# Optimization experiments

Hardware: AMD Instinct MI355X
Metric: run time of the kernel (lower is better)

The kernel has to match this reference:

```python
import jax, jax.numpy as jnp
import numpy as np
from jax import lax

B, L, V = 128, 64, 8192
E = H = 128
STEPS = 10
MAX_BIN = 512
BETA_START, BETA_END = 1e-4, 2e-2


def setup_inputs():
    key = jax.random.key(0)
    k = jax.random.split(key, 23)
    s = 0.05
    padded_x = (jax.random.uniform(k[0], (B, L, V)) < 0.01).astype(jnp.float32)
    lengths = jax.random.randint(k[1], (B,), 1, L + 1)
    visit_mask = (jnp.arange(L)[None, :] < lengths[:, None]).astype(jnp.float32)
    padded_bins = jnp.sort(jax.random.randint(k[2], (B, L), 0, MAX_BIN), axis=1)
    t_diff = jax.random.randint(k[3], (B,), 1, STEPS + 1)
    eps = jax.random.normal(k[4], (B, L, E))
    z0 = jax.random.normal(k[5], (B, L, E))
    noise = jax.random.normal(k[6], (STEPS, B, L, E))
    W_visit = jax.random.normal(k[7], (E, V)) * s
    bin_embed = (jax.random.normal(k[8], (MAX_BIN + 2, E)) * s).at[0].set(0.0)  # padding_idx=0
    W_ih = jax.random.normal(k[9], (4 * H, E)) * s
    W_hh = jax.random.normal(k[10], (4 * H, H)) * s
    b_ih = jax.random.normal(k[11], (4 * H,)) * s
    b_hh = jax.random.normal(k[12], (4 * H,)) * s
    W_cls = jax.random.normal(k[13], (1, H)) * s
    b_cls = jax.random.normal(k[14], (1,)) * s
    W_proj = jax.random.normal(k[15], (E, H)) * s
    time_embed = jax.random.normal(k[16], (STEPS + 1, E)) * s
    W_fuse = jax.random.normal(k[17], (2, 2 * E)) * s
    b_fuse = jax.random.normal(k[18], (2,)) * s
    W_e1 = jax.random.normal(k[19], (E, 2 * E)) * s
    b_e1 = jax.random.normal(k[20], (E,)) * s
    W_e2 = jax.random.normal(k[21], (E, E)) * s
    b_e2 = jax.random.normal(k[22], (E,)) * s
    return dict(padded_x=padded_x, visit_mask=visit_mask, padded_bins=padded_bins,
                t_diff=t_diff, eps=eps, z0=z0, noise=noise, W_visit=W_visit,
                bin_embed=bin_embed, W_ih=W_ih, W_hh=W_hh, b_ih=b_ih, b_hh=b_hh,
                W_cls=W_cls, b_cls=b_cls, W_proj=W_proj, time_embed=time_embed,
                W_fuse=W_fuse, b_fuse=b_fuse, W_e1=W_e1, b_e1=b_e1, W_e2=W_e2, b_e2=b_e2)


def _lstm(v, W_ih, W_hh, b_ih, b_hh):
    # v: [B,L,E] -> h: [B,L,H]; PyTorch gate order i,f,g,o
    xg = jnp.einsum('ble,ge->blg', v, W_ih) + b_ih + b_hh
    def step(carry, x):
        h, c = carry
        g = x + h @ W_hh.T
        i, f, gg, o = jnp.split(g, 4, axis=-1)
        c = jax.nn.sigmoid(f) * c + jax.nn.sigmoid(i) * jnp.tanh(gg)
        h = jax.nn.sigmoid(o) * jnp.tanh(c)
        return (h, c), h
    z = jnp.zeros((v.shape[0], W_hh.shape[1]), v.dtype)
    _, hs = lax.scan(step, (z, z), jnp.swapaxes(xg, 0, 1))
    return jnp.swapaxes(hs, 0, 1)


def _last_hidden(h, mask):
    lengths = jnp.maximum(mask.sum(axis=1).astype(jnp.int32), 1)
    return h[jnp.arange(h.shape[0]), lengths - 1]


def reference(padded_x, visit_mask, padded_bins, t_diff, eps, z0, noise,
              W_visit, bin_embed, W_ih, W_hh, b_ih, b_hh, W_cls, b_cls,
              W_proj, time_embed, W_fuse, b_fuse, W_e1, b_e1, W_e2, b_e2):
    m = visit_mask[..., None]                      # [B,L,1]
    betas = jnp.linspace(BETA_START, BETA_END, STEPS)
    alphas = 1.0 - betas
    alpha_bars = jnp.cumprod(alphas)

    # visit embedding + time-gap (delta bin) embedding
    delta = jnp.concatenate([jnp.zeros_like(padded_bins[:, :1]),
                             jnp.clip(padded_bins[:, 1:] - padded_bins[:, :-1], 0)], axis=1)
    delta = jnp.where(visit_mask > 0, jnp.clip(delta, 0, MAX_BIN + 1), 0)
    v = (padded_x @ W_visit.T + bin_embed[delta]) * m  # [B,L,E]

    # encoder LSTM (packed seq == plain scan then zero padded suffix positions)
    h = _lstm(v, W_ih, W_hh, b_ih, b_hh) * m
    logits_real = (_last_hidden(h, visit_mask) @ W_cls.T + b_cls)[:, 0]

    h_prev = jnp.pad(h[:, :-1], ((0, 0), (1, 0), (0, 0)))
    hp = (h_prev @ W_proj.T) * m                   # [B,L,E]

    def fuse_eps(z, t_emb):
        a = jax.nn.softmax(jnp.concatenate([z, hp], -1) @ W_fuse.T + b_fuse, axis=-1)
        g = a[..., :1] * z + a[..., 1:] * hp
        x = jnp.concatenate([g, t_emb], -1)
        return jax.nn.relu(x @ W_e1.T + b_e1) @ W_e2.T + b_e2

    # diffusion loss
    t = jnp.where(visit_mask > 0, t_diff[:, None], 1)    # [B,L]
    ab = alpha_bars[t - 1][..., None]
    z_t = (jnp.sqrt(ab) * v + jnp.sqrt(1.0 - ab) * eps) * m
    eps_pred = fuse_eps(z_t, time_embed[t])
    denom = jnp.maximum(visit_mask.sum(), 1.0)
    diffusion_loss = jnp.sum((eps_pred - eps) ** 2 * m) / denom

    # reverse diffusion sampling of synthetic visit embeddings
    def step(z, inp):
        kk, nz = inp
        t_s = jnp.where(visit_mask > 0, kk, 1)
        e = fuse_eps(z, time_embed[t_s])
        beta = betas[kk - 1]
        mean = (z - beta / jnp.sqrt(1.0 - alpha_bars[kk - 1]) * e) / jnp.sqrt(alphas[kk - 1])
        z = jnp.where(kk > 1, mean + jnp.sqrt(beta) * nz, mean) * m
        return z, None

    ks = jnp.arange(STEPS, 0, -1)
    v_syn, _ = lax.scan(step, z0, (ks, noise))

    h_syn = _lstm(v_syn, W_ih, W_hh, b_ih, b_hh) * m
    logits_syn = (_last_hidden(h_syn, visit_mask) @ W_cls.T + b_cls)[:, 0]
    return logits_real, logits_syn, diffusion_loss
```

## Files before the change

kernel.cpp:

```cpp
#include <hip/hip_runtime.h>

#define B_ 128
#define L_ 64
#define V_ 8192
#define E_ 128
#define H_ 128
#define NROW (B_*L_)
#define HSTRIDE 136
#define AS 136
#define XS 264
#define YS 136
#define ZS 132
#define HS2 136

typedef unsigned short u16;
typedef __attribute__((ext_vector_type(8))) short bf16x8;
typedef __attribute__((ext_vector_type(4))) float f32x4;

__device__ __forceinline__ float sigm(float x){ return 1.f/(1.f + __expf(-x)); }
__device__ __forceinline__ float ftanh(float x){ float e = __expf(2.f*x); return 1.f - 2.f/(e + 1.f); }
__device__ __forceinline__ u16 f2bf(float f){
    union { unsigned int i; float f; } x; x.f = f;
    unsigned int r = x.i + 0x7fff + ((x.i >> 16) & 1);
    return (u16)(r >> 16);
}
#define LBAR() asm volatile("s_waitcnt lgkmcnt(0)\ns_barrier" ::: "memory")

__device__ __forceinline__ bf16x8 pack8(const float* p){
    const float4* q = (const float4*)p;
    float4 a = q[0], b = q[1];
    bf16x8 f;
    f[0]=(short)f2bf(a.x); f[1]=(short)f2bf(a.y); f[2]=(short)f2bf(a.z); f[3]=(short)f2bf(a.w);
    f[4]=(short)f2bf(b.x); f[5]=(short)f2bf(b.y); f[6]=(short)f2bf(b.z); f[7]=(short)f2bf(b.w);
    return f;
}

__global__ __launch_bounds__(256) void k_transpose_wv(const float* __restrict__ Wv, float* __restrict__ WT){
    __shared__ float tile[16][129];
    int v0 = blockIdx.x * 16;
    int t = threadIdx.x;
    #pragma unroll
    for(int i=0;i<8;i++){
        int idx = i*256 + t; int e = idx >> 4; int vv = idx & 15;
        tile[vv][e] = Wv[(size_t)e*V_ + v0 + vv];
    }
    __syncthreads();
    #pragma unroll
    for(int i=0;i<8;i++){
        int idx = i*256 + t; int vv = idx >> 7; int e = idx & 127;
        WT[(size_t)(v0+vv)*E_ + e] = tile[vv][e];
    }
}

__global__ __launch_bounds__(256) void k_visit_embed(const float* __restrict__ px, const float* __restrict__ vmask,
                                                     const int* __restrict__ bins, const float* __restrict__ bemb,
                                                     const float* __restrict__ WT, float* __restrict__ v){
    __shared__ int idxs[512];
    __shared__ int cnt;
    __shared__ int dsh;
    __shared__ float msh;
    __shared__ float4 red[8][32];
    int row = blockIdx.x; int l = row & 63;
    int t = threadIdx.x;
    if(t==0){
        cnt = 0;
        float m = vmask[row];
        int d = 0;
        if(l > 0){ d = bins[row] - bins[row-1]; d = d < 0 ? 0 : (d > 513 ? 513 : d); }
        if(!(m > 0.f)) d = 0;
        dsh = d; msh = m;
    }
    __syncthreads();
    const uint4* xr4 = (const uint4*)(px + (size_t)row * V_);
    for(int i=t;i<2048;i+=256){
        uint4 u = xr4[i];
        unsigned int w[4] = {u.x,u.y,u.z,u.w};
        #pragma unroll
        for(int j=0;j<4;j++){
            if(w[j]){ int p = atomicAdd(&cnt,1); if(p<512) idxs[p] = i*4 + j; }
        }
    }
    __syncthreads();
    int n = cnt; if(n > 512) n = 512;
    int eq = t & 31, jg = t >> 5;
    float4 a4 = {0.f,0.f,0.f,0.f};
    for(int j=jg;j<n;j+=8){
        const float4* wr = (const float4*)(WT + (size_t)idxs[j]*E_);
        float4 wv = wr[eq];
        a4.x += wv.x; a4.y += wv.y; a4.z += wv.z; a4.w += wv.w;
    }
    red[jg][eq] = a4;
    __syncthreads();
    if(t < 32){
        float4 s = red[0][t];
        #pragma unroll
        for(int g=1;g<8;g++){
            float4 r = red[g][t];
            s.x += r.x; s.y += r.y; s.z += r.z; s.w += r.w;
        }
        const float4* bp = (const float4*)(bemb + dsh*E_);
        float4 bv = bp[t];
        float m = msh;
        float4 o;
        o.x = (s.x + bv.x)*m; o.y = (s.y + bv.y)*m; o.z = (s.z + bv.z)*m; o.w = (s.w + bv.w)*m;
        ((float4*)(v + (size_t)row*E_))[t] = o;
    }
}

__global__ __launch_bounds__(256) void k_pack(const float* __restrict__ Whh, const float* __restrict__ Wih,
                                              const float* __restrict__ We1, const float* __restrict__ We2,
                                              const float* __restrict__ Wproj,
                                              u16* __restrict__ dWhh, u16* __restrict__ dWih,
                                              u16* __restrict__ dWe1, u16* __restrict__ dWe2,
                                              u16* __restrict__ dWproj){
    int bid = blockIdx.x; int t = threadIdx.x;
    const float* src; u16* dst; int WS,TS,NT,KT,K; int base;
    if(bid<32){ src=Whh; dst=dWhh; WS=16; TS=128; NT=4; KT=4; K=128; base=bid; }
    else if(bid<64){ src=Wih; dst=dWih; WS=128; TS=16; NT=8; KT=4; K=128; base=bid-32; }
    else if(bid<80){ src=We1; dst=dWe1; WS=32; TS=16; NT=2; KT=8; K=256; base=bid-64; }
    else if(bid<88){ src=We2; dst=dWe2; WS=32; TS=16; NT=2; KT=4; K=128; base=bid-80; }
    else { src=Wproj; dst=dWproj; WS=32; TS=16; NT=2; KT=4; K=128; base=bid-88; }
    for(int i=0;i<8;i++){
        int o = base*2048 + i*256 + t;
        int g = o >> 9; int lane = (o >> 3) & 63; int j = o & 7;
        int kt = g % KT; int r2 = g / KT; int nt = r2 % NT; int w = r2 / NT;
        int lc = lane & 15; int quad = lane >> 4;
        int n = w*WS + nt*TS + lc; int k = kt*32 + quad*8 + j;
        dst[o] = f2bf(src[(size_t)n*K + k]);
    }
}

__global__ __launch_bounds__(256,2) void k_gemm_xgp(const float* __restrict__ A, const u16* __restrict__ Wihp,
                                                    const float* __restrict__ bih, const float* __restrict__ bhh,
                                                    float* __restrict__ xgp){
    __shared__ __align__(16) u16 abuf[16*AS];
    int t = threadIdx.x, wave = t >> 6, lane = t & 63, quad = lane >> 4, lc = lane & 15;
    int bid = blockIdx.x; int bg = bid >> 6, l = bid & 63;
    #pragma unroll
    for(int i=0;i<8;i++){
        int flat = i*256 + t; int r = flat >> 7, e = flat & 127;
        abuf[r*AS + e] = f2bf(A[((size_t)(bg*16+r)*64 + l)*E_ + e]);
    }
    bf16x8 wg[8][4]; float bb[8];
    #pragma unroll
    for(int nt=0;nt<8;nt++){
        int n = wave*128 + nt*16 + lc;
        bb[nt] = bih[n] + bhh[n];
        #pragma unroll
        for(int kt=0;kt<4;kt++)
            wg[nt][kt] = *(const bf16x8*)(Wihp + (((wave*8+nt)*4+kt)<<9) + lane*8);
    }
    __syncthreads();
    f32x4 ac[8];
    #pragma unroll
    for(int nt=0;nt<8;nt++) ac[nt] = (f32x4){0.f,0.f,0.f,0.f};
    #pragma unroll
    for(int kt=0;kt<4;kt++){
        bf16x8 af = *(const bf16x8*)&abuf[lc*AS + kt*32 + quad*8];
        #pragma unroll
        for(int nt=0;nt<8;nt++)
            ac[nt] = __builtin_amdgcn_mfma_f32_16x16x32_bf16(af, wg[nt][kt], ac[nt], 0,0,0);
    }
    float* dst = xgp + (size_t)bid*8192;
    #pragma unroll
    for(int nt=0;nt<8;nt++){
        float4 o;
        o.x = ac[nt][0] + bb[nt]; o.y = ac[nt][1] + bb[nt];
        o.z = ac[nt][2] + bb[nt]; o.w = ac[nt][3] + bb[nt];
        *(float4*)(dst + nt*1024 + quad*256 + lc*16 + wave*4) = o;
    }
}

template<bool STOREH>
__device__ __forceinline__ void lstm_step(int l,
        const u16* __restrict__ bufr, u16* __restrict__ bufw,
        const f32x4*& pxg, u16* hsp,
        const bf16x8 (&bfh)[4][4],
        f32x4 (&xc)[4], f32x4 (&xn)[4], float (&c4)[4], float (&lg4)[4],
        const int (&len4)[4], float wcv, int lc, int quad, int cw){
    if(l+1 < 64){
        #pragma unroll
        for(int g=0;g<4;g++) xn[g] = pxg[g];
        pxg += 2048;
    }
    bf16x8 afh[4];
    #pragma unroll
    for(int kt=0;kt<4;kt++)
        afh[kt] = *(const bf16x8*)&bufr[lc*HSTRIDE + kt*32 + quad*8];
    f32x4 acc[4];
    #pragma unroll
    for(int g=0;g<4;g++) acc[g] = (f32x4){0.f,0.f,0.f,0.f};
    #pragma unroll
    for(int kt=0;kt<4;kt++){
        #pragma unroll
        for(int g=0;g<4;g++)
            acc[g] = __builtin_amdgcn_mfma_f32_16x16x32_bf16(afh[kt], bfh[g][kt], acc[g], 0,0,0);
    }
    #pragma unroll
    for(int r=0;r<4;r++){
        float gi = acc[0][r] + xc[0][r];
        float gf = acc[1][r] + xc[1][r];
        float gg = acc[2][r] + xc[2][r];
        float go = acc[3][r] + xc[3][r];
        float c  = sigm(gf)*c4[r] + sigm(gi)*ftanh(gg);
        float h  = sigm(go)*ftanh(c);
        c4[r] = c;
        u16 hb = f2bf(h);
        bufw[(quad*4+r)*HSTRIDE + cw] = hb;
        if constexpr (STOREH) hsp[(size_t)r*8192 + (size_t)l*128] = hb;
        if(l == len4[r]-1) lg4[r] += h * wcv;
    }
    LBAR();
}

template<bool STOREH>
__global__ __attribute__((amdgpu_waves_per_eu(2,2))) __launch_bounds__(512)
void k_lstm(const float* __restrict__ xgp, const u16* __restrict__ Whhp,
            const float* __restrict__ Wcls, const float* __restrict__ bcls,
            const float* __restrict__ vmask, u16* __restrict__ h_store,
            float* __restrict__ logits_out){
    __shared__ __align__(16) u16 hbuf[2][16*HSTRIDE];
    __shared__ float vmsh[16*64];
    __shared__ int lensh[16];
    __shared__ float lgsh[16][132];
    int t = threadIdx.x;
    int wave = t >> 6, lane = t & 63;
    int quad = lane >> 4, lc = lane & 15;
    int cw = wave*16 + lc;
    int bg = blockIdx.x; int b0 = bg * 16;

    for(int i=t;i<16*HSTRIDE;i+=512) hbuf[0][i] = 0;
    for(int i=t;i<1024;i+=512) vmsh[i] = vmask[b0*64 + i];
    __syncthreads();
    if(t < 16){
        int s = 0;
        #pragma unroll
        for(int i=0;i<64;i++) s += (vmsh[t*64 + i] > 0.f) ? 1 : 0;
        lensh[t] = s < 1 ? 1 : s;
    }

    bf16x8 bfh[4][4];
    #pragma unroll
    for(int g=0;g<4;g++)
        #pragma unroll
        for(int kt=0;kt<4;kt++)
            bfh[g][kt] = *(const bf16x8*)(Whhp + (((wave*4+g)*4+kt)<<9) + lane*8);
    float wcv = Wcls[cw];
    float c4[4] = {0.f,0.f,0.f,0.f};
    float lg4[4] = {0.f,0.f,0.f,0.f};
    u16* hsp = STOREH ? (h_store + ((size_t)(b0 + quad*4)*64)*128 + cw) : (u16*)nullptr;

    const f32x4* pxg = (const f32x4*)(xgp + (size_t)bg*64*8192) + t*4;
    f32x4 x0[4], x1[4];
    #pragma unroll
    for(int g=0;g<4;g++) x0[g] = pxg[g];
    pxg += 2048;
    __syncthreads();
    int len4[4];
    #pragma unroll
    for(int r=0;r<4;r++) len4[r] = lensh[quad*4 + r];

    for(int lb=0;lb<64;lb+=2){
        lstm_step<STOREH>(lb,   hbuf[0], hbuf[1], pxg, hsp, bfh, x0, x1, c4, lg4, len4, wcv, lc, quad, cw);
        lstm_step<STOREH>(lb+1, hbuf[1], hbuf[0], pxg, hsp, bfh, x1, x0, c4, lg4, len4, wcv, lc, quad, cw);
    }
    #pragma unroll
    for(int r=0;r<4;r++) lgsh[quad*4+r][cw] = lg4[r];
    __syncthreads();
    {
        int row = t >> 5, l32 = t & 31;
        float s = lgsh[row][l32] + lgsh[row][l32+32] + lgsh[row][l32+64] + lgsh[row][l32+96];
        s += __shfl_down(s, 16, 32);
        s += __shfl_down(s, 8, 32);
        s += __shfl_down(s, 4, 32);
        s += __shfl_down(s, 2, 32);
        s += __shfl_down(s, 1, 32);
        if(l32 == 0) logits_out[b0 + row] = s + bcls[0];
    }
}

__global__ __launch_bounds__(256,2) void k_drg(const float* __restrict__ v, const u16* __restrict__ h,
        const float* __restrict__ eps, const int* __restrict__ tdiff, const float* __restrict__ vmask,
        const float* __restrict__ z0, const float* __restrict__ noise, const float* __restrict__ temb,
        const float* __restrict__ Wf, const float* __restrict__ bfu,
        const u16* __restrict__ We1p, const float* __restrict__ be1,
        const u16* __restrict__ We2p, const float* __restrict__ be2,
        const u16* __restrict__ Wprojp,
        float* __restrict__ partial, float* __restrict__ vsyn){
    __shared__ __align__(16) float zbuf[16*ZS];
    __shared__ float hpbuf[16*ZS];
    __shared__ __align__(16) u16 xbuf[16*XS];
    __shared__ __align__(16) u16 y1buf[16*YS];
    __shared__ __align__(16) u16 hb16[16*HS2];
    __shared__ float wfsh[512];
    __shared__ float ssh[16][2], hpd[16][2];
    __shared__ float mrow[16]; __shared__ int trow[16];
    __shared__ float sbeta[10], sabar[10];
    __shared__ float rb[4];
    int row0 = blockIdx.x * 16; int t = threadIdx.x;
    int wave = t >> 6, lane = t & 63, quad = lane >> 4, lc = lane & 15;

    if(t==0){
        float p = 1.f;
        for(int k=0;k<10;k++){ float b = 1e-4f + (0.02f - 1e-4f)*k/9.f; sbeta[k] = b; p *= (1.f - b); sabar[k] = p; }
    }
    if(t < 16){
        int row = row0 + t; float m = vmask[row];
        mrow[t] = m; trow[t] = (m > 0.f) ? tdiff[row >> 6] : 1;
    }
    for(int i=t;i<512;i+=256) wfsh[i] = Wf[i];
    __syncthreads();
    #pragma unroll
    for(int i=0;i<8;i++){
        int flat = i*256 + t; int r = flat >> 7; int e = flat & 127; int row = row0 + r;
        float ab = sabar[trow[r]-1];
        zbuf[r*ZS + e] = (sqrtf(ab)*v[(size_t)row*E_ + e] + sqrtf(1.f - ab)*eps[(size_t)row*E_ + e]) * mrow[r];
    }
    {
        int r = t >> 4, e0 = (t & 15) * 8;
        bf16x8 hv;
        if(((row0 & 63) == 0) && r == 0){
            hv = (bf16x8){0,0,0,0,0,0,0,0};
        } else {
            hv = *(const bf16x8*)(h + (size_t)(row0 - 1 + r)*E_ + e0);
        }
        *(bf16x8*)&hb16[r*HS2 + e0] = hv;
    }
    bf16x8 wf1[2][8], wf2[2][4], pf[2][4];
    float be1v[2], be2v[2];
    #pragma unroll
    for(int nt=0;nt<2;nt++){
        int n = wave*32 + nt*16 + lc;
        be1v[nt] = be1[n]; be2v[nt] = be2[n];
        #pragma unroll
        for(int kt=0;kt<8;kt++) wf1[nt][kt] = *(const bf16x8*)(We1p + (((wave*2+nt)*8+kt)<<9) + lane*8);
        #pragma unroll
        for(int kt=0;kt<4;kt++){
            wf2[nt][kt] = *(const bf16x8*)(We2p + (((wave*2+nt)*4+kt)<<9) + lane*8);
            pf[nt][kt]  = *(const bf16x8*)(Wprojp + (((wave*2+nt)*4+kt)<<9) + lane*8);
        }
    }
    __syncthreads();
    {
        f32x4 ap[2];
        ap[0] = (f32x4){0.f,0.f,0.f,0.f}; ap[1] = (f32x4){0.f,0.f,0.f,0.f};
        #pragma unroll
        for(int kt=0;kt<4;kt++){
            bf16x8 af = *(const bf16x8*)&hb16[lc*HS2 + kt*32 + quad*8];
            ap[0] = __builtin_amdgcn_mfma_f32_16x16x32_bf16(af, pf[0][kt], ap[0], 0,0,0);
            ap[1] = __builtin_amdgcn_mfma_f32_16x16x32_bf16(af, pf[1][kt], ap[1], 0,0,0);
        }
        #pragma unroll
        for(int nt=0;nt<2;nt++)
            #pragma unroll
            for(int rr=0;rr<4;rr++)
                hpbuf[(quad*4+rr)*ZS + wave*32 + nt*16 + lc] = ap[nt][rr];
    }
    __syncthreads();
    {
        int row = t >> 4, k = (t >> 3) & 1, sub = t & 7;
        float p = 0.f;
        #pragma unroll
        for(int i=0;i<16;i++)
            p += hpbuf[row*ZS + sub*16 + i] * wfsh[k*256 + 128 + sub*16 + i];
        p += __shfl_down(p,4); p += __shfl_down(p,2); p += __shfl_down(p,1);
        if(sub == 0) hpd[row][k] = p + bfu[k];
    }
    __syncthreads();

    for(int s=0;s<11;s++){
        int kk = 11 - s;
        float nzv[8], epv[8], z0v[8];
        if(s >= 1){
            #pragma unroll
            for(int nt=0;nt<2;nt++)
                #pragma unroll
                for(int r=0;r<4;r++)
                    nzv[nt*4+r] = noise[((size_t)(s-1)*NROW + row0 + quad*4 + r)*E_ + wave*32 + nt*16 + lc];
        } else {
            #pragma unroll
            for(int nt=0;nt<2;nt++)
                #pragma unroll
                for(int r=0;r<4;r++)
                    epv[nt*4+r] = eps[(size_t)(row0 + quad*4 + r)*E_ + wave*32 + nt*16 + lc];
            #pragma unroll
            for(int i=0;i<8;i++){
                int flat = i*256 + t;
                z0v[i] = z0[(size_t)(row0 + (flat >> 7))*E_ + (flat & 127)];
            }
        }
        {
            int row = t >> 4, k = (t >> 3) & 1, sub = t & 7;
            float q = 0.f;
            #pragma unroll
            for(int i=0;i<16;i++)
                q += zbuf[row*ZS + sub*16 + i] * wfsh[k*256 + sub*16 + i];
            q += __shfl_down(q,4); q += __shfl_down(q,2); q += __shfl_down(q,1);
            if(sub == 0) ssh[row][k] = q + hpd[row][k];
        }
        __syncthreads();
        {
            int row = t >> 4, c0 = (t & 15) * 16;
            float s0 = ssh[row][0], s1 = ssh[row][1];
            float a0 = 1.f/(1.f + __expf(s1 - s0)), a1 = 1.f - a0;
            int tt = (s == 0) ? trow[row] : ((mrow[row] > 0.f) ? kk : 1);
            #pragma unroll
            for(int i=0;i<16;i++){
                int c = c0 + i;
                float val = (c < 128) ? (a0*zbuf[row*ZS + c] + a1*hpbuf[row*ZS + c])
                                      : temb[tt*E_ + (c - 128)];
                xbuf[row*XS + c] = f2bf(val);
            }
        }
        __syncthreads();
        f32x4 acc1[2];
        acc1[0] = (f32x4){0.f,0.f,0.f,0.f}; acc1[1] = (f32x4){0.f,0.f,0.f,0.f};
        #pragma unroll
        for(int kt=0;kt<8;kt++){
            bf16x8 af = *(const bf16x8*)&xbuf[lc*XS + kt*32 + quad*8];
            acc1[0] = __builtin_amdgcn_mfma_f32_16x16x32_bf16(af, wf1[0][kt], acc1[0], 0,0,0);
            acc1[1] = __builtin_amdgcn_mfma_f32_16x16x32_bf16(af, wf1[1][kt], acc1[1], 0,0,0);
        }
        #pragma unroll
        for(int nt=0;nt<2;nt++){
            #pragma unroll
            for(int r=0;r<4;r++)
                y1buf[(quad*4+r)*YS + wave*32 + nt*16 + lc] = f2bf(fmaxf(acc1[nt][r] + be1v[nt], 0.f));
        }
        __syncthreads();
        f32x4 acc2[2];
        acc2[0] = (f32x4){0.f,0.f,0.f,0.f}; acc2[1] = (f32x4){0.f,0.f,0.f,0.f};
        #pragma unroll
        for(int kt=0;kt<4;kt++){
            bf16x8 af = *(const bf16x8*)&y1buf[lc*YS + kt*32 + quad*8];
            acc2[0] = __builtin_amdgcn_mfma_f32_16x16x32_bf16(af, wf2[0][kt], acc2[0], 0,0,0);
            acc2[1] = __builtin_amdgcn_mfma_f32_16x16x32_bf16(af, wf2[1][kt], acc2[1], 0,0,0);
        }
        if(s == 0){
            float lp = 0.f;
            #pragma unroll
            for(int nt=0;nt<2;nt++){
                #pragma unroll
                for(int r=0;r<4;r++){
                    int m = quad*4 + r;
                    float d = (acc2[nt][r] + be2v[nt]) - epv[nt*4+r];
                    lp += d*d*mrow[m];
                }
            }
            #pragma unroll
            for(int off=32;off;off>>=1) lp += __shfl_down(lp, off);
            if(lane == 0) rb[wave] = lp;
            __syncthreads();
            if(t == 0) partial[blockIdx.x] = rb[0]+rb[1]+rb[2]+rb[3];
            #pragma unroll
            for(int i=0;i<8;i++){
                int flat = i*256 + t; int r = flat >> 7; int e = flat & 127;
                zbuf[r*ZS + e] = z0v[i];
            }
            __syncthreads();
        } else {
            float beta = sbeta[kk-1];
            float c1 = beta / sqrtf(1.f - sabar[kk-1]);
            float c2 = 1.f / sqrtf(1.f - beta);
            float sb = sqrtf(beta);
            #pragma unroll
            for(int nt=0;nt<2;nt++){
                int n = wave*32 + nt*16 + lc;
                #pragma unroll
                for(int r=0;r<4;r++){
                    int m = quad*4 + r;
                    float e = acc2[nt][r] + be2v[nt];
                    float z = zbuf[m*ZS + n];
                    float mean = (z - c1*e) * c2;
                    float nz = nzv[nt*4+r];
                    float znew = (kk > 1) ? (mean + sb*nz) : mean;
                    zbuf[m*ZS + n] = znew * mrow[m];
                }
            }
            __syncthreads();
        }
    }
    {
        int r = t >> 4, e0 = (t & 15) * 8;
        float4 a = *(const float4*)&zbuf[r*ZS + e0];
        float4 b2 = *(const float4*)&zbuf[r*ZS + e0 + 4];
        *(float4*)&vsyn[(size_t)(row0 + r)*E_ + e0] = a;
        *(float4*)&vsyn[(size_t)(row0 + r)*E_ + e0 + 4] = b2;
    }
}

__global__ void k_finalize(const float* __restrict__ partial, const float* __restrict__ vmask, float* __restrict__ out){
    __shared__ float rb[4], rl[4];
    int t = threadIdx.x;
    float s = 0.f;
    for(int i=t;i<NROW;i+=256) s += vmask[i];
    float ls = 0.f;
    for(int i=t;i<512;i+=256) ls += partial[i];
    #pragma unroll
    for(int off=32;off;off>>=1){ s += __shfl_down(s, off); ls += __shfl_down(ls, off); }
    if((t & 63) == 0){ rb[t >> 6] = s; rl[t >> 6] = ls; }
    __syncthreads();
    if(t == 0){
        float denom = rb[0]+rb[1]+rb[2]+rb[3];
        if(denom < 1.f) denom = 1.f;
        out[256] = (rl[0]+rl[1]+rl[2]+rl[3]) / denom;
    }
}

extern "C" void kernel_launch(void* const* d_in, const int* in_sizes, int n_in,
                              void* d_out, int out_size, void* d_ws, size_t ws_size,
                              hipStream_t stream){
    const float* px    = (const float*)d_in[0];
    const float* vmask = (const float*)d_in[1];
    const int*   bins  = (const int*)d_in[2];
    const int*   tdiff = (const int*)d_in[3];
    const float* eps   = (const float*)d_in[4];
    const float* z0    = (const float*)d_in[5];
    const float* noise = (const float*)d_in[6];
    const float* Wv    = (const float*)d_in[7];
    const float* bemb  = (const float*)d_in[8];
    const float* Wih   = (const float*)d_in[9];
    const float* Whh   = (const float*)d_in[10];
    const float* bih   = (const float*)d_in[11];
    const float* bhh   = (const float*)d_in[12];
    const float* Wcls  = (const float*)d_in[13];
    const float* bcls  = (const float*)d_in[14];
    const float* Wproj = (const float*)d_in[15];
    const float* temb  = (const float*)d_in[16];
    const float* Wf    = (const float*)d_in[17];
    const float* bfu   = (const float*)d_in[18];
    const float* We1   = (const float*)d_in[19];
    const float* be1   = (const float*)d_in[20];
    const float* We2   = (const float*)d_in[21];
    const float* be2   = (const float*)d_in[22];
    float* out = (float*)d_out;

    float* ws = (float*)d_ws;
    float* xgp     = ws;
    float* WT      = ws + 4194304;
    u16*  Whh_p    = (u16*)(ws + 4194304);
    u16*  Wih_p    = (u16*)(ws + 4227072);
    u16*  We1_p    = (u16*)(ws + 4259840);
    u16*  We2_p    = (u16*)(ws + 4276224);
    u16*  Wproj_p  = (u16*)(ws + 4284416);
    u16*  h_store  = (u16*)(ws + 4292608);
    float* v       = ws + 5242880;
    float* vsyn    = ws + 6291456;
    float* partial = ws + 7340032;

    hipLaunchKernelGGL(k_transpose_wv, dim3(V_/16), dim3(256), 0, stream, Wv, WT);
    hipLaunchKernelGGL(k_visit_embed, dim3(NROW), dim3(256), 0, stream, px, vmask, bins, bemb, WT, v);
    hipLaunchKernelGGL(k_pack, dim3(96), dim3(256), 0, stream, Whh, Wih, We1, We2, Wproj,
                       Whh_p, Wih_p, We1_p, We2_p, Wproj_p);
    hipLaunchKernelGGL(k_gemm_xgp, dim3(512), dim3(256), 0, stream, v, Wih_p, bih, bhh, xgp);
    hipLaunchKernelGGL((k_lstm<true>), dim3(B_/16), dim3(512), 0, stream,
                       xgp, Whh_p, Wcls, bcls, vmask, h_store, out);
    hipLaunchKernelGGL(k_drg, dim3(NROW/16), dim3(256), 0, stream,
                       v, h_store, eps, tdiff, vmask, z0, noise, temb, Wf, bfu,
                       We1_p, be1, We2_p, be2, Wproj_p, partial, vsyn);
    hipLaunchKernelGGL(k_gemm_xgp, dim3(512), dim3(256), 0, stream, vsyn, Wih_p, bih, bhh, xgp);
    hipLaunchKernelGGL((k_lstm<false>), dim3(B_/16), dim3(512), 0, stream,
                       xgp, Whh_p, Wcls, bcls, vmask, (u16*)nullptr, out + 128);
    hipLaunchKernelGGL(k_finalize, dim3(1), dim3(256), 0, stream, partial, vmask, out);
}
```

Baseline: 742.3 us.

## Merge weight transpose and pack kernels, batch visit loads, two timesteps per GEMM block

The Wv transpose and the bf16 weight packing now run as one launch, with the packed buffers moved to a workspace region that does not overlap WT. The visit-embedding kernel issues all eight 16-byte loads of a row before scanning them, which raises memory-level parallelism. The xgp GEMM has each block handle two timesteps so the preloaded Wih fragments are reused and the grid is halved. The costs are fewer blocks for the GEMM, more LDS per block and more registers held for the batched loads.

```diff
diff --git a/kernel.cpp b/kernel.cpp
--- a/kernel.cpp
+++ b/kernel.cpp
@@ -35,20 +35,44 @@
     return f;
 }
 
-__global__ __launch_bounds__(256) void k_transpose_wv(const float* __restrict__ Wv, float* __restrict__ WT){
+__global__ __launch_bounds__(256) void k_prep(const float* __restrict__ Wv, float* __restrict__ WT,
+                                              const float* __restrict__ Whh, const float* __restrict__ Wih,
+                                              const float* __restrict__ We1, const float* __restrict__ We2,
+                                              const float* __restrict__ Wproj,
+                                              u16* __restrict__ dWhh, u16* __restrict__ dWih,
+                                              u16* __restrict__ dWe1, u16* __restrict__ dWe2,
+                                              u16* __restrict__ dWproj){
     __shared__ float tile[16][129];
-    int v0 = blockIdx.x * 16;
     int t = threadIdx.x;
-    #pragma unroll
+    if(blockIdx.x < 512){
+        int v0 = blockIdx.x * 16;
+        #pragma unroll
+        for(int i=0;i<8;i++){
+            int idx = i*256 + t; int e = idx >> 4; int vv = idx & 15;
+            tile[vv][e] = Wv[(size_t)e*V_ + v0 + vv];
+        }
+        __syncthreads();
+        #pragma unroll
+        for(int i=0;i<8;i++){
+            int idx = i*256 + t; int vv = idx >> 7; int e = idx & 127;
+            WT[(size_t)(v0+vv)*E_ + e] = tile[vv][e];
+        }
+        return;
+    }
+    int bid = blockIdx.x - 512;
+    const float* src; u16* dst; int WS,TS,NT,KT,K; int base;
+    if(bid<32){ src=Whh; dst=dWhh; WS=16; TS=128; NT=4; KT=4; K=128; base=bid; }
+    else if(bid<64){ src=Wih; dst=dWih; WS=128; TS=16; NT=8; KT=4; K=128; base=bid-32; }
+    else if(bid<80){ src=We1; dst=dWe1; WS=32; TS=16; NT=2; KT=8; K=256; base=bid-64; }
+    else if(bid<88){ src=We2; dst=dWe2; WS=32; TS=16; NT=2; KT=4; K=128; base=bid-80; }
+    else { src=Wproj; dst=dWproj; WS=32; TS=16; NT=2; KT=4; K=128; base=bid-88; }
     for(int i=0;i<8;i++){
-        int idx = i*256 + t; int e = idx >> 4; int vv = idx & 15;
-        tile[vv][e] = Wv[(size_t)e*V_ + v0 + vv];
-    }
-    __syncthreads();
-    #pragma unroll
-    for(int i=0;i<8;i++){
-        int idx = i*256 + t; int vv = idx >> 7; int e = idx & 127;
-        WT[(size_t)(v0+vv)*E_ + e] = tile[vv][e];
+        int o = base*2048 + i*256 + t;
+        int g = o >> 9; int lane = (o >> 3) & 63; int j = o & 7;
+        int kt = g % KT; int r2 = g / KT; int nt = r2 % NT; int w = r2 / NT;
+        int lc = lane & 15; int quad = lane >> 4;
+        int n = w*WS + nt*TS + lc; int k = kt*32 + quad*8 + j;
+        dst[o] = f2bf(src[(size_t)n*K + k]);
     }
 }
 
@@ -72,12 +96,15 @@
     }
     __syncthreads();
     const uint4* xr4 = (const uint4*)(px + (size_t)row * V_);
-    for(int i=t;i<2048;i+=256){
-        uint4 u = xr4[i];
-        unsigned int w[4] = {u.x,u.y,u.z,u.w};
+    uint4 u8[8];
+    #pragma unroll
+    for(int i=0;i<8;i++) u8[i] = xr4[t + i*256];
+    #pragma unroll
+    for(int i=0;i<8;i++){
+        unsigned int w[4] = {u8[i].x,u8[i].y,u8[i].z,u8[i].w};
         #pragma unroll
         for(int j=0;j<4;j++){
-            if(w[j]){ int p = atomicAdd(&cnt,1); if(p<512) idxs[p] = i*4 + j; }
+            if(w[j]){ int p = atomicAdd(&cnt,1); if(p<512) idxs[p] = (t + i*256)*4 + j; }
         }
     }
     __syncthreads();
@@ -107,39 +134,16 @@
     }
 }
 
-__global__ __launch_bounds__(256) void k_pack(const float* __restrict__ Whh, const float* __restrict__ Wih,
-                                              const float* __restrict__ We1, const float* __restrict__ We2,
-                                              const float* __restrict__ Wproj,
-                                              u16* __restrict__ dWhh, u16* __restrict__ dWih,
-                                              u16* __restrict__ dWe1, u16* __restrict__ dWe2,
-                                              u16* __restrict__ dWproj){
-    int bid = blockIdx.x; int t = threadIdx.x;
-    const float* src; u16* dst; int WS,TS,NT,KT,K; int base;
-    if(bid<32){ src=Whh; dst=dWhh; WS=16; TS=128; NT=4; KT=4; K=128; base=bid; }
-    else if(bid<64){ src=Wih; dst=dWih; WS=128; TS=16; NT=8; KT=4; K=128; base=bid-32; }
-    else if(bid<80){ src=We1; dst=dWe1; WS=32; TS=16; NT=2; KT=8; K=256; base=bid-64; }
-    else if(bid<88){ src=We2; dst=dWe2; WS=32; TS=16; NT=2; KT=4; K=128; base=bid-80; }
-    else { src=Wproj; dst=dWproj; WS=32; TS=16; NT=2; KT=4; K=128; base=bid-88; }
-    for(int i=0;i<8;i++){
-        int o = base*2048 + i*256 + t;
-        int g = o >> 9; int lane = (o >> 3) & 63; int j = o & 7;
-        int kt = g % KT; int r2 = g / KT; int nt = r2 % NT; int w = r2 / NT;
-        int lc = lane & 15; int quad = lane >> 4;
-        int n = w*WS + nt*TS + lc; int k = kt*32 + quad*8 + j;
-        dst[o] = f2bf(src[(size_t)n*K + k]);
-    }
-}
-
 __global__ __launch_bounds__(256,2) void k_gemm_xgp(const float* __restrict__ A, const u16* __restrict__ Wihp,
                                                     const float* __restrict__ bih, const float* __restrict__ bhh,
                                                     float* __restrict__ xgp){
-    __shared__ __align__(16) u16 abuf[16*AS];
+    __shared__ __align__(16) u16 abuf[2][16*AS];
     int t = threadIdx.x, wave = t >> 6, lane = t & 63, quad = lane >> 4, lc = lane & 15;
-    int bid = blockIdx.x; int bg = bid >> 6, l = bid & 63;
-    #pragma unroll
-    for(int i=0;i<8;i++){
-        int flat = i*256 + t; int r = flat >> 7, e = flat & 127;
-        abuf[r*AS + e] = f2bf(A[((size_t)(bg*16+r)*64 + l)*E_ + e]);
+    int bid = blockIdx.x; int bg = bid >> 5, l0 = (bid & 31)*2;
+    #pragma unroll
+    for(int i=0;i<16;i++){
+        int flat = i*256 + t; int s = flat >> 11; int r = (flat >> 7) & 15; int e = flat & 127;
+        abuf[s][r*AS + e] = f2bf(A[((size_t)(bg*16+r)*64 + l0 + s)*E_ + e]);
     }
     bf16x8 wg[8][4]; float bb[8];
     #pragma unroll
@@ -151,23 +155,26 @@
             wg[nt][kt] = *(const bf16x8*)(Wihp + (((wave*8+nt)*4+kt)<<9) + lane*8);
     }
     __syncthreads();
-    f32x4 ac[8];
-    #pragma unroll
-    for(int nt=0;nt<8;nt++) ac[nt] = (f32x4){0.f,0.f,0.f,0.f};
-    #pragma unroll
-    for(int kt=0;kt<4;kt++){
-        bf16x8 af = *(const bf16x8*)&abuf[lc*AS + kt*32 + quad*8];
-        #pragma unroll
-        for(int nt=0;nt<8;nt++)
-            ac[nt] = __builtin_amdgcn_mfma_f32_16x16x32_bf16(af, wg[nt][kt], ac[nt], 0,0,0);
-    }
-    float* dst = xgp + (size_t)bid*8192;
-    #pragma unroll
-    for(int nt=0;nt<8;nt++){
-        float4 o;
-        o.x = ac[nt][0] + bb[nt]; o.y = ac[nt][1] + bb[nt];
-        o.z = ac[nt][2] + bb[nt]; o.w = ac[nt][3] + bb[nt];
-        *(float4*)(dst + nt*1024 + quad*256 + lc*16 + wave*4) = o;
+    #pragma unroll
+    for(int s=0;s<2;s++){
+        f32x4 ac[8];
+        #pragma unroll
+        for(int nt=0;nt<8;nt++) ac[nt] = (f32x4){0.f,0.f,0.f,0.f};
+        #pragma unroll
+        for(int kt=0;kt<4;kt++){
+            bf16x8 af = *(const bf16x8*)&abuf[s][lc*AS + kt*32 + quad*8];
+            #pragma unroll
+            for(int nt=0;nt<8;nt++)
+                ac[nt] = __builtin_amdgcn_mfma_f32_16x16x32_bf16(af, wg[nt][kt], ac[nt], 0,0,0);
+        }
+        float* dst = xgp + (size_t)(bg*64 + l0 + s)*8192;
+        #pragma unroll
+        for(int nt=0;nt<8;nt++){
+            float4 o;
+            o.x = ac[nt][0] + bb[nt]; o.y = ac[nt][1] + bb[nt];
+            o.z = ac[nt][2] + bb[nt]; o.w = ac[nt][3] + bb[nt];
+            *(float4*)(dst + nt*1024 + quad*256 + lc*16 + wave*4) = o;
+        }
     }
 }
 
@@ -538,27 +545,26 @@
     float* ws = (float*)d_ws;
     float* xgp     = ws;
     float* WT      = ws + 4194304;
-    u16*  Whh_p    = (u16*)(ws + 4194304);
-    u16*  Wih_p    = (u16*)(ws + 4227072);
-    u16*  We1_p    = (u16*)(ws + 4259840);
-    u16*  We2_p    = (u16*)(ws + 4276224);
-    u16*  Wproj_p  = (u16*)(ws + 4284416);
-    u16*  h_store  = (u16*)(ws + 4292608);
     float* v       = ws + 5242880;
     float* vsyn    = ws + 6291456;
     float* partial = ws + 7340032;
-
-    hipLaunchKernelGGL(k_transpose_wv, dim3(V_/16), dim3(256), 0, stream, Wv, WT);
+    u16*  Whh_p    = (u16*)(ws + 7340544);
+    u16*  Wih_p    = Whh_p + 65536;
+    u16*  We1_p    = Whh_p + 131072;
+    u16*  We2_p    = Whh_p + 163840;
+    u16*  Wproj_p  = Whh_p + 180224;
+    u16*  h_store  = (u16*)(ws + 7438848);
+
+    hipLaunchKernelGGL(k_prep, dim3(608), dim3(256), 0, stream, Wv, WT,
+                       Whh, Wih, We1, We2, Wproj, Whh_p, Wih_p, We1_p, We2_p, Wproj_p);
     hipLaunchKernelGGL(k_visit_embed, dim3(NROW), dim3(256), 0, stream, px, vmask, bins, bemb, WT, v);
-    hipLaunchKernelGGL(k_pack, dim3(96), dim3(256), 0, stream, Whh, Wih, We1, We2, Wproj,
-                       Whh_p, Wih_p, We1_p, We2_p, Wproj_p);
-    hipLaunchKernelGGL(k_gemm_xgp, dim3(512), dim3(256), 0, stream, v, Wih_p, bih, bhh, xgp);
+    hipLaunchKernelGGL(k_gemm_xgp, dim3(256), dim3(256), 0, stream, v, Wih_p, bih, bhh, xgp);
     hipLaunchKernelGGL((k_lstm<true>), dim3(B_/16), dim3(512), 0, stream,
                        xgp, Whh_p, Wcls, bcls, vmask, h_store, out);
     hipLaunchKernelGGL(k_drg, dim3(NROW/16), dim3(256), 0, stream,
                        v, h_store, eps, tdiff, vmask, z0, noise, temb, Wf, bfu,
                        We1_p, be1, We2_p, be2, Wproj_p, partial, vsyn);
-    hipLaunchKernelGGL(k_gemm_xgp, dim3(512), dim3(256), 0, stream, vsyn, Wih_p, bih, bhh, xgp);
+    hipLaunchKernelGGL(k_gemm_xgp, dim3(256), dim3(256), 0, stream, vsyn, Wih_p, bih, bhh, xgp);
     hipLaunchKernelGGL((k_lstm<false>), dim3(B_/16), dim3(512), 0, stream,
                        xgp, Whh_p, Wcls, bcls, vmask, (u16*)nullptr, out + 128);
     hipLaunchKernelGGL(k_finalize, dim3(1), dim3(256), 0, stream, partial, vmask, out);
```

Result: faster. 725.4 us (-2.3%).
